# Optimization experiments

Measured on AMD Instinct MI355X. Metric: run time of the kernel, lower is better.

Reference implementation:

```python
import jax, jax.numpy as jnp
import numpy as np
from jax import lax

C = 256
HEADS = 8
HEAD_DIM = C // HEADS
B, H, W = 16, 32, 32
EPS = 1e-5


def conv3x3(x, w, b):
    # x: [B,C,H,W], w: [O,I,3,3]
    y = lax.conv_general_dilated(x, w, (1, 1), 'SAME',
                                 dimension_numbers=('NCHW', 'OIHW', 'NCHW'))
    return y + b[None, :, None, None]


def conv1x1(x, w, b):
    # w: [O,C]; pointwise conv as einsum
    return jnp.einsum('oc,bchw->bohw', w, x) + b[None, :, None, None]


def batchnorm(x, gamma, beta, mean, var):
    inv = gamma / jnp.sqrt(var + EPS)
    return x * inv[None, :, None, None] + (beta - mean * inv)[None, :, None, None]


def setup_inputs() -> dict:
    key = jax.random.key(0)
    ks = jax.random.split(key, 16)
    s3 = 1.0 / np.sqrt(C * 9)
    s1 = 1.0 / np.sqrt(C)
    return {
        'x': jax.random.normal(ks[0], (B, C, H, W), jnp.float32),
        'conv1_w': jax.random.normal(ks[1], (C, C, 3, 3), jnp.float32) * s3,
        'conv1_b': jnp.zeros((C,), jnp.float32),
        'bn1_gamma': jnp.ones((C,), jnp.float32),
        'bn1_beta': jnp.zeros((C,), jnp.float32),
        'bn1_mean': jax.random.normal(ks[2], (C,), jnp.float32) * 0.1,
        'bn1_var': jax.random.uniform(ks[3], (C,), jnp.float32, 0.5, 1.5),
        'conv2_w': jax.random.normal(ks[4], (C, C, 3, 3), jnp.float32) * s3,
        'conv2_b': jnp.zeros((C,), jnp.float32),
        'bn2_gamma': jnp.ones((C,), jnp.float32),
        'bn2_beta': jnp.zeros((C,), jnp.float32),
        'bn2_mean': jax.random.normal(ks[5], (C,), jnp.float32) * 0.1,
        'bn2_var': jax.random.uniform(ks[6], (C,), jnp.float32, 0.5, 1.5),
        'q_w': jax.random.normal(ks[7], (C, C), jnp.float32) * s1,
        'q_b': jnp.zeros((C,), jnp.float32),
        'k_w': jax.random.normal(ks[8], (C, C), jnp.float32) * s1,
        'k_b': jnp.zeros((C,), jnp.float32),
        'v_w': jax.random.normal(ks[9], (C, C), jnp.float32) * s1,
        'v_b': jnp.zeros((C,), jnp.float32),
        'out_w': jax.random.normal(ks[10], (C, C), jnp.float32) * s1,
        'out_b': jnp.zeros((C,), jnp.float32),
        'gate': jnp.asarray(0.1, jnp.float32),
    }


def reference(x, conv1_w, conv1_b, bn1_gamma, bn1_beta, bn1_mean, bn1_var,
              conv2_w, conv2_b, bn2_gamma, bn2_beta, bn2_mean, bn2_var,
              q_w, q_b, k_w, k_b, v_w, v_b, out_w, out_b, gate):
    b, c, h, w = x.shape
    n = h * w
    residual = x
    # conv residual path
    conv_out = jax.nn.relu(batchnorm(conv3x3(x, conv1_w, conv1_b),
                                     bn1_gamma, bn1_beta, bn1_mean, bn1_var))
    conv_out = batchnorm(conv3x3(conv_out, conv2_w, conv2_b),
                         bn2_gamma, bn2_beta, bn2_mean, bn2_var)
    # spatial multi-head attention (eval mode: dropout is identity)
    q = conv1x1(x, q_w, q_b).reshape(b, HEADS, HEAD_DIM, n)
    k = conv1x1(x, k_w, k_b).reshape(b, HEADS, HEAD_DIM, n)
    v = conv1x1(x, v_w, v_b).reshape(b, HEADS, HEAD_DIM, n)
    scores = jnp.einsum('bhdn,bhdm->bhnm', q, k) / np.sqrt(HEAD_DIM).astype(np.float32)
    attn = jax.nn.softmax(scores, axis=-1)  # [B,heads,N,N]
    attn_out = jnp.einsum('bhdm,bhnm->bhdn', v, attn).reshape(b, c, h, w)
    attn_out = conv1x1(attn_out, out_w, out_b)
    out = conv_out + jax.nn.sigmoid(gate) * attn_out + residual
    return jax.nn.relu(out)
```

## Files before the change

kernel.cpp:

```cpp
#include <hip/hip_runtime.h>
#include <hip/hip_bf16.h>

using bf16 = __hip_bfloat16;
typedef __attribute__((ext_vector_type(4))) float floatx4;
typedef __attribute__((ext_vector_type(8))) __bf16 bf16x8;
typedef __attribute__((ext_vector_type(4))) __bf16 bf16x4;

#define LGKM_WAIT() asm volatile("s_waitcnt lgkmcnt(0)" ::: "memory")

__device__ __forceinline__ void prep_one(const float* __restrict__ src,
                                         bf16* __restrict__ dst, int idx, int ntaps)
{
    const int kk = idx & 31, o = (idx >> 5) & 255, kc = (idx >> 13) & 7, t = idx >> 16;
    dst[idx] = __float2bfloat16(src[(o * 256 + kc * 32 + kk) * ntaps + t]);
}

__global__ __launch_bounds__(256) void prep_all(
    const float* __restrict__ x, const float* __restrict__ w1,
    const float* __restrict__ qw, const float* __restrict__ kw,
    const float* __restrict__ vw, const float* __restrict__ ow,
    bf16* __restrict__ xk, bf16* __restrict__ w1f,
    bf16* __restrict__ qwf, bf16* __restrict__ kwf,
    bf16* __restrict__ vwf, bf16* __restrict__ owf)
{
    __shared__ float T[64][65];
    const int blk = blockIdx.x, tid = threadIdx.x;
    if (blk < 1024) {
        const int n0 = (blk & 15) * 64, c0 = ((blk >> 4) & 3) * 64, b = blk >> 6;
        #pragma unroll
        for (int it = 0; it < 4; ++it) {
            const int tau = tid + it * 256;
            const int c = tau >> 4, seg = tau & 15;
            const float4 vv = *(const float4*)&x[((b * 256 + c0 + c) << 10) + n0 + seg * 4];
            T[seg * 4 + 0][c] = vv.x; T[seg * 4 + 1][c] = vv.y;
            T[seg * 4 + 2][c] = vv.z; T[seg * 4 + 3][c] = vv.w;
        }
        __syncthreads();
        #pragma unroll
        for (int it = 0; it < 2; ++it) {
            const int tau = tid + it * 256;
            const int n = tau >> 3, seg = tau & 7;
            bf16x8 o8;
            #pragma unroll
            for (int q = 0; q < 8; ++q) o8[q] = (__bf16)T[n][seg * 8 + q];
            const int c = c0 + seg * 8;
            *(bf16x8*)&xk[((((b << 3) + (c >> 5)) << 10) + n0 + n) * 32 + (c & 31)] = o8;
        }
    } else if (blk < 1600) {
        const int base = (blk - 1024) * 1024 + tid;
        #pragma unroll
        for (int k = 0; k < 4; ++k) prep_one(w1, w1f, base + k * 256, 9);
    } else {
        const int r = (blk - 1600) * 256 + tid;
        prep_one(qw, qwf, r, 1);
        prep_one(kw, kwf, r, 1);
        prep_one(vw, vwf, r, 1);
        prep_one(ow, owf, r, 1);
    }
}

template<int MODE>
__device__ __forceinline__ void conv_body(
    unsigned char* smb, int bn, int bo, int b,
    const bf16* __restrict__ Wf, const bf16* __restrict__ Act,
    const float* __restrict__ bias,
    const float* __restrict__ gam, const float* __restrict__ bet,
    const float* __restrict__ mu, const float* __restrict__ var,
    void* __restrict__ outp)
{
    const int tid = threadIdx.x;
    const int wave = tid >> 6, lane = tid & 63;
    const int quad = lane >> 4, l16 = lane & 15;
    const int wm = wave & 1, wn = wave >> 1;

    int srow[4], scol[4], sn[4]; bool sval[4];
    #pragma unroll
    for (int it = 0; it < 4; ++it) {
        const int s = tid + it * 256;
        const int row = s >> 2;
        const int yi = row / 34, x34 = row - yi * 34;
        const int gy = bn * 4 - 1 + yi, gx = x34 - 1;
        sval[it] = (s < 816) & (gy >= 0) & (gy < 32) & (gx >= 0) & (gx < 32);
        sn[it] = (gy << 5) + gx;
        srow[it] = row; scol[it] = (s & 3) * 8;
    }

    const bf16* __restrict__ act0 = Act + ((size_t)b << 18);
    bf16x8 rg[4];
    #pragma unroll
    for (int it = 0; it < 4; ++it) {
        bf16x8 v = {};
        if (sval[it]) v = *(const bf16x8*)&act0[sn[it] * 32 + scol[it]];
        rg[it] = v;
    }
    {
        bf16* st = (bf16*)smb;
        #pragma unroll
        for (int it = 0; it < 4; ++it)
            if (tid + it * 256 < 816) *(bf16x8*)&st[srow[it] * 40 + scol[it]] = rg[it];
    }
    __syncthreads();

    floatx4 acc[4][2] = {};

    for (int kc = 0; kc < 8; ++kc) {
        if (kc < 7) {
            const bf16* __restrict__ actn = act0 + ((kc + 1) << 15);
            #pragma unroll
            for (int it = 0; it < 4; ++it) {
                bf16x8 v = {};
                if (sval[it]) v = *(const bf16x8*)&actn[sn[it] * 32 + scol[it]];
                rg[it] = v;
            }
        }
        const bf16* __restrict__ cur = (const bf16*)(smb + (kc & 1) * 16320);
        #pragma unroll
        for (int t = 0; t < 9; ++t) {
            const int dy = t / 3 - 1, dx = t % 3 - 1;
            bf16x8 af[4], wf[2];
            #pragma unroll
            for (int p = 0; p < 4; ++p) {
                const int m = wm * 64 + p * 16 + l16;
                const int row = ((m >> 5) + 1 + dy) * 34 + ((m & 31) + 1 + dx);
                af[p] = *(const bf16x8*)&cur[row * 40 + quad * 8];
            }
            #pragma unroll
            for (int p = 0; p < 2; ++p)
                wf[p] = *(const bf16x8*)&Wf[((((t * 8 + kc) << 8) + bo * 64 + wn * 32 + p * 16 + l16) << 5) + quad * 8];
            #pragma unroll
            for (int i = 0; i < 4; ++i)
                #pragma unroll
                for (int j = 0; j < 2; ++j)
                    acc[i][j] = __builtin_amdgcn_mfma_f32_16x16x32_bf16(af[i], wf[j], acc[i][j], 0, 0, 0);
        }
        if (kc < 7) {
            bf16* nxt = (bf16*)(smb + ((kc + 1) & 1) * 16320);
            #pragma unroll
            for (int it = 0; it < 4; ++it)
                if (tid + it * 256 < 816) *(bf16x8*)&nxt[srow[it] * 40 + scol[it]] = rg[it];
        }
        __syncthreads();
    }

    if constexpr (MODE == 0) {
        bf16* rp = (bf16*)(smb + wave * 5120);
        #pragma unroll
        for (int i = 0; i < 4; ++i)
            #pragma unroll
            for (int j = 0; j < 2; ++j) {
                const int oc = bo * 64 + wn * 32 + j * 16 + l16;
                const float inv = gam[oc] * rsqrtf(var[oc] + 1e-5f);
                const float sh = bet[oc] - mu[oc] * inv;
                const float bs = bias[oc];
                #pragma unroll
                for (int r = 0; r < 4; ++r) {
                    const float v = (acc[i][j][r] + bs) * inv + sh;
                    rp[(i * 16 + quad * 4 + r) * 40 + j * 16 + l16] =
                        __float2bfloat16(v < 0.0f ? 0.0f : v);
                }
            }
        LGKM_WAIT();
        const int kc2 = bo * 2 + wn;
        bf16* dst = (bf16*)outp + ((((size_t)b << 3) + kc2) << 15) + (bn * 128 + wm * 64) * 32;
        #pragma unroll
        for (int it = 0; it < 4; ++it) {
            const int s = it * 64 + lane;
            const int nl = s >> 2, cp = (s & 3) * 8;
            *(bf16x8*)&dst[nl * 32 + cp] = *(const bf16x8*)&rp[nl * 40 + cp];
        }
    } else {
        float* rp = (float*)(smb + wave * 8704);
        #pragma unroll
        for (int i = 0; i < 4; ++i)
            #pragma unroll
            for (int j = 0; j < 2; ++j) {
                const int oc = bo * 64 + wn * 32 + j * 16 + l16;
                const float inv = gam[oc] * rsqrtf(var[oc] + 1e-5f);
                const float sh = bet[oc] - mu[oc] * inv;
                const float bs = bias[oc];
                float4 o;
                o.x = (acc[i][j][0] + bs) * inv + sh;
                o.y = (acc[i][j][1] + bs) * inv + sh;
                o.z = (acc[i][j][2] + bs) * inv + sh;
                o.w = (acc[i][j][3] + bs) * inv + sh;
                *(float4*)&rp[(j * 16 + l16) * 68 + i * 16 + quad * 4] = o;
            }
        LGKM_WAIT();
        const int n0 = bn * 128 + wm * 64;
        #pragma unroll
        for (int it = 0; it < 8; ++it) {
            const int s = it * 64 + lane;
            const int ocl = s >> 4, nch = s & 15;
            const int oc = bo * 64 + wn * 32 + ocl;
            float4 v = *(const float4*)&rp[ocl * 68 + nch * 4];
            *(float4*)&((float*)outp)[((b * 256 + oc) << 10) + n0 + nch * 4] = v;
        }
    }
}

__device__ __forceinline__ void qkv_body(
    unsigned char* qsm, int bn, int by, int b,
    const bf16* __restrict__ Wq, const bf16* __restrict__ Wk, const bf16* __restrict__ Wv,
    const bf16* __restrict__ Act,
    const float* __restrict__ bq, const float* __restrict__ bk, const float* __restrict__ bv,
    bf16* __restrict__ Oq, bf16* __restrict__ Ok, bf16* __restrict__ Ov, float qscale)
{
    const int sel = by >> 2, bo = by & 3;
    const bf16* __restrict__ Wf = (sel == 0) ? Wq : (sel == 1) ? Wk : Wv;
    const float* __restrict__ bias = (sel == 0) ? bq : (sel == 1) ? bk : bv;
    const float scale = (sel == 0) ? qscale : 1.0f;

    const int tid = threadIdx.x;
    const int wave = tid >> 6, lane = tid & 63;
    const int quad = lane >> 4, l16 = lane & 15;
    const int wm = wave & 1, wn = wave >> 1;

    floatx4 acc[4][2] = {};

    for (int kc = 0; kc < 8; ++kc) {
        const bf16* __restrict__ actk = Act + ((size_t)b << 18) + (kc << 15);
        bf16x8 af[4], wf[2];
        #pragma unroll
        for (int p = 0; p < 4; ++p)
            af[p] = *(const bf16x8*)&actk[(bn * 128 + wm * 64 + p * 16 + l16) * 32 + quad * 8];
        #pragma unroll
        for (int p = 0; p < 2; ++p)
            wf[p] = *(const bf16x8*)&Wf[(((kc << 8) + bo * 64 + wn * 32 + p * 16 + l16) << 5) + quad * 8];
        #pragma unroll
        for (int i = 0; i < 4; ++i)
            #pragma unroll
            for (int j = 0; j < 2; ++j)
                acc[i][j] = __builtin_amdgcn_mfma_f32_16x16x32_bf16(af[i], wf[j], acc[i][j], 0, 0, 0);
    }

    if (sel < 2) {
        bf16* rp = (bf16*)(qsm + wave * 5120);
        #pragma unroll
        for (int i = 0; i < 4; ++i)
            #pragma unroll
            for (int j = 0; j < 2; ++j) {
                const int oc = bo * 64 + wn * 32 + j * 16 + l16;
                const float bs = bias[oc];
                #pragma unroll
                for (int r = 0; r < 4; ++r)
                    rp[(i * 16 + quad * 4 + r) * 40 + j * 16 + l16] =
                        __float2bfloat16((acc[i][j][r] + bs) * scale);
            }
        LGKM_WAIT();
        bf16* __restrict__ outp = (sel == 0) ? Oq : Ok;
        const int h = bo * 2 + wn;
        bf16* dst = outp + ((((size_t)b << 3) + h) << 15) + (bn * 128 + wm * 64) * 32;
        #pragma unroll
        for (int it = 0; it < 4; ++it) {
            const int s = it * 64 + lane;
            const int nl = s >> 2, cp = (s & 3) * 8;
            *(bf16x8*)&dst[nl * 32 + cp] = *(const bf16x8*)&rp[nl * 40 + cp];
        }
    } else {
        #pragma unroll
        for (int i = 0; i < 4; ++i)
            #pragma unroll
            for (int j = 0; j < 2; ++j) {
                const int oc = bo * 64 + wn * 32 + j * 16 + l16;
                const int h = oc >> 5, d = oc & 31;
                const float bs = bias[oc];
                bf16x4 o4;
                #pragma unroll
                for (int r = 0; r < 4; ++r) o4[r] = (__bf16)(acc[i][j][r] + bs);
                const int key = bn * 128 + wm * 64 + i * 16 + quad * 4;
                *(bf16x4*)&Ov[(((((size_t)b << 3) + h) * 32 + (key >> 5)) * 32 + d) * 32 + (key & 31)] = o4;
            }
    }
}

__device__ __forceinline__ void attn_body(
    unsigned char* smb, int L,
    const bf16* __restrict__ Q, const bf16* __restrict__ K,
    const bf16* __restrict__ V, bf16* __restrict__ O)
{
    bf16 (*Pl)[32][136] = (bf16 (*)[32][136])smb;

    const int h = L & 7, slot = L >> 3;
    const int b = slot & 15, qb = slot >> 4;
    const int tid = threadIdx.x;
    const int wave = tid >> 6, lane = tid & 63;
    const int quad = lane >> 4, l16 = lane & 15;

    const bf16* __restrict__ Qh = Q + ((((size_t)b << 3) + h) << 15);
    const bf16* __restrict__ Kh = K + ((((size_t)b << 3) + h) << 15);
    const bf16* __restrict__ Vh = V + ((((size_t)b << 3) + h) << 15);
    const int qrow0 = qb * 128 + wave * 32;

    bf16x8 qf[2];
    #pragma unroll
    for (int i = 0; i < 2; ++i)
        qf[i] = *(const bf16x8*)&Qh[(qrow0 + i * 16 + l16) * 32 + quad * 8];

    float lp[2] = {0.0f, 0.0f};
    floatx4 oacc[2][2] = {};

    for (int kt = 0; kt < 8; ++kt) {
        bf16x8 kf[8];
        #pragma unroll
        for (int kb = 0; kb < 8; ++kb)
            kf[kb] = *(const bf16x8*)&Kh[(kt * 128 + kb * 16 + l16) * 32 + quad * 8];
        bf16x8 vb[2][4];
        #pragma unroll
        for (int jd = 0; jd < 2; ++jd)
            #pragma unroll
            for (int kk = 0; kk < 4; ++kk)
                vb[jd][kk] = *(const bf16x8*)&Vh[(((kt * 4 + kk) << 5) + jd * 16 + l16) * 32 + quad * 8];

        #pragma unroll
        for (int kb = 0; kb < 8; ++kb) {
            #pragma unroll
            for (int i = 0; i < 2; ++i) {
                floatx4 zz = {0.f, 0.f, 0.f, 0.f};
                floatx4 st = __builtin_amdgcn_mfma_f32_16x16x32_bf16(kf[kb], qf[i], zz, 0, 0, 0);
                const float e0 = __builtin_amdgcn_exp2f(st[0]);
                const float e1 = __builtin_amdgcn_exp2f(st[1]);
                const float e2 = __builtin_amdgcn_exp2f(st[2]);
                const float e3 = __builtin_amdgcn_exp2f(st[3]);
                lp[i] += (e0 + e1) + (e2 + e3);
                bf16x4 p4 = {(__bf16)e0, (__bf16)e1, (__bf16)e2, (__bf16)e3};
                *(bf16x4*)&Pl[wave][i * 16 + l16][kb * 16 + quad * 4] = p4;
            }
        }

        #pragma unroll
        for (int kk = 0; kk < 4; ++kk) {
            bf16x8 pf[2];
            #pragma unroll
            for (int i = 0; i < 2; ++i)
                pf[i] = *(const bf16x8*)&Pl[wave][i * 16 + l16][kk * 32 + quad * 8];
            #pragma unroll
            for (int jd = 0; jd < 2; ++jd)
                #pragma unroll
                for (int i = 0; i < 2; ++i)
                    oacc[jd][i] = __builtin_amdgcn_mfma_f32_16x16x32_bf16(
                        vb[jd][kk], pf[i], oacc[jd][i], 0, 0, 0);
        }
    }

    bf16* __restrict__ Oh = O + ((((size_t)b << 3) + h) << 15);
    #pragma unroll
    for (int i = 0; i < 2; ++i) {
        float l = lp[i];
        l += __shfl_xor(l, 16, 64);
        l += __shfl_xor(l, 32, 64);
        const float inv = 1.0f / l;
        const int qn = qrow0 + i * 16 + l16;
        #pragma unroll
        for (int jd = 0; jd < 2; ++jd) {
            bf16x4 o4;
            #pragma unroll
            for (int r = 0; r < 4; ++r) o4[r] = (__bf16)(oacc[jd][i][r] * inv);
            *(bf16x4*)&Oh[qn * 32 + jd * 16 + quad * 4] = o4;
        }
    }
}

__global__ __launch_bounds__(256) void phase1_k(
    const bf16* __restrict__ w1f, const bf16* __restrict__ xk,
    const float* __restrict__ cb1,
    const float* __restrict__ g1, const float* __restrict__ be1,
    const float* __restrict__ mu1, const float* __restrict__ va1,
    bf16* __restrict__ y1k,
    const bf16* __restrict__ qwf, const bf16* __restrict__ kwf, const bf16* __restrict__ vwf,
    const float* __restrict__ qb_, const float* __restrict__ kb_, const float* __restrict__ vb_,
    bf16* __restrict__ qT, bf16* __restrict__ kT, bf16* __restrict__ vbuf, float qscale,
    const float* __restrict__ w2, bf16* __restrict__ w2f)
{
    __shared__ __align__(16) unsigned char smb[34816];
    const int L = blockIdx.x;
    if (L < 512) {
        const int bn = L & 7, bo = (L >> 3) & 3, b = L >> 5;
        conv_body<0>(smb, bn, bo, b, w1f, xk, cb1, g1, be1, mu1, va1, (void*)y1k);
    } else if (L < 2048) {
        const int L2 = L - 512;
        const int bn = L2 & 7, by = (L2 >> 3) % 12, b = L2 / 96;
        qkv_body(smb, bn, by, b, qwf, kwf, vwf, xk, qb_, kb_, vb_, qT, kT, vbuf, qscale);
    } else {
        const int base = (L - 2048) * 1024 + threadIdx.x;
        #pragma unroll
        for (int k = 0; k < 4; ++k) prep_one(w2, w2f, base + k * 256, 9);
    }
}

__global__ __launch_bounds__(256) void phase2_k(
    const bf16* __restrict__ w2f, const bf16* __restrict__ y1k,
    const float* __restrict__ cb2,
    const float* __restrict__ g2, const float* __restrict__ be2,
    const float* __restrict__ mu2, const float* __restrict__ va2,
    float* __restrict__ c2,
    const bf16* __restrict__ qT, const bf16* __restrict__ kT,
    const bf16* __restrict__ vbuf, bf16* __restrict__ attnk)
{
    __shared__ __align__(16) unsigned char smb[34816];
    const int L = blockIdx.x;
    if (L < 512) {
        const int bn = L & 7, bo = (L >> 3) & 3, b = L >> 5;
        conv_body<1>(smb, bn, bo, b, w2f, y1k, cb2, g2, be2, mu2, va2, (void*)c2);
    } else {
        attn_body(smb, L - 512, qT, kT, vbuf, attnk);
    }
}

__global__ __launch_bounds__(256) void fi_k(
    const bf16* __restrict__ Wf, const bf16* __restrict__ Act,
    const float* __restrict__ bias,
    const float* __restrict__ c2, const float* __restrict__ resid,
    const float* __restrict__ gate, float* __restrict__ outp)
{
    __shared__ __align__(16) unsigned char fsm[34816];
    const int bn = blockIdx.x, bo = blockIdx.y, b = blockIdx.z;
    const int tid = threadIdx.x;
    const int wave = tid >> 6, lane = tid & 63;
    const int quad = lane >> 4, l16 = lane & 15;
    const int wm = wave & 1, wn = wave >> 1;

    floatx4 acc[4][2] = {};

    for (int kc = 0; kc < 8; ++kc) {
        const bf16* __restrict__ actk = Act + ((size_t)b << 18) + (kc << 15);
        bf16x8 af[4], wf[2];
        #pragma unroll
        for (int p = 0; p < 4; ++p)
            af[p] = *(const bf16x8*)&actk[(bn * 128 + wm * 64 + p * 16 + l16) * 32 + quad * 8];
        #pragma unroll
        for (int p = 0; p < 2; ++p)
            wf[p] = *(const bf16x8*)&Wf[(((kc << 8) + bo * 64 + wn * 32 + p * 16 + l16) << 5) + quad * 8];
        #pragma unroll
        for (int i = 0; i < 4; ++i)
            #pragma unroll
            for (int j = 0; j < 2; ++j)
                acc[i][j] = __builtin_amdgcn_mfma_f32_16x16x32_bf16(af[i], wf[j], acc[i][j], 0, 0, 0);
    }

    const float sg = 1.0f / (1.0f + __expf(-gate[0]));

    float* rp = (float*)(fsm + wave * 8704);
    #pragma unroll
    for (int i = 0; i < 4; ++i)
        #pragma unroll
        for (int j = 0; j < 2; ++j) {
            const int oc = bo * 64 + wn * 32 + j * 16 + l16;
            const float bs = bias[oc];
            float4 o;
            o.x = acc[i][j][0] + bs; o.y = acc[i][j][1] + bs;
            o.z = acc[i][j][2] + bs; o.w = acc[i][j][3] + bs;
            *(float4*)&rp[(j * 16 + l16) * 68 + i * 16 + quad * 4] = o;
        }
    LGKM_WAIT();
    const int n0 = bn * 128 + wm * 64;
    #pragma unroll
    for (int it = 0; it < 8; ++it) {
        const int s = it * 64 + lane;
        const int ocl = s >> 4, nch = s & 15;
        const int oc = bo * 64 + wn * 32 + ocl;
        const int idx = ((b * 256 + oc) << 10) + n0 + nch * 4;
        float4 v = *(const float4*)&rp[ocl * 68 + nch * 4];
        const float4 cc = *(const float4*)&c2[idx];
        const float4 rr = *(const float4*)&resid[idx];
        float4 o;
        o.x = cc.x + sg * v.x + rr.x; o.y = cc.y + sg * v.y + rr.y;
        o.z = cc.z + sg * v.z + rr.z; o.w = cc.w + sg * v.w + rr.w;
        o.x = o.x < 0.0f ? 0.0f : o.x; o.y = o.y < 0.0f ? 0.0f : o.y;
        o.z = o.z < 0.0f ? 0.0f : o.z; o.w = o.w < 0.0f ? 0.0f : o.w;
        *(float4*)&outp[idx] = o;
    }
}

extern "C" void kernel_launch(void* const* d_in, const int* in_sizes, int n_in,
                              void* d_out, int out_size, void* d_ws, size_t ws_size,
                              hipStream_t stream)
{
    const float* x    = (const float*)d_in[0];
    const float* w1   = (const float*)d_in[1];
    const float* cb1  = (const float*)d_in[2];
    const float* g1   = (const float*)d_in[3];
    const float* be1  = (const float*)d_in[4];
    const float* mu1  = (const float*)d_in[5];
    const float* va1  = (const float*)d_in[6];
    const float* w2   = (const float*)d_in[7];
    const float* cb2  = (const float*)d_in[8];
    const float* g2   = (const float*)d_in[9];
    const float* be2  = (const float*)d_in[10];
    const float* mu2  = (const float*)d_in[11];
    const float* va2  = (const float*)d_in[12];
    const float* qw   = (const float*)d_in[13];
    const float* qb_  = (const float*)d_in[14];
    const float* kw   = (const float*)d_in[15];
    const float* kb_  = (const float*)d_in[16];
    const float* vw   = (const float*)d_in[17];
    const float* vb_  = (const float*)d_in[18];
    const float* ow   = (const float*)d_in[19];
    const float* ob_  = (const float*)d_in[20];
    const float* gate = (const float*)d_in[21];

    char* ws = (char*)d_ws;
    bf16*  xk    = (bf16*) (ws + 0);
    bf16*  y1k   = (bf16*) (ws + 8388608);
    bf16*  attnk = (bf16*) (ws + 8388608);
    float* c2    = (float*)(ws + 16777216);
    bf16*  qT    = (bf16*) (ws + 33554432);
    bf16*  kT    = (bf16*) (ws + 41943040);
    bf16*  vbuf  = (bf16*) (ws + 50331648);
    bf16*  w1f   = (bf16*) (ws + 58720256);
    bf16*  w2f   = (bf16*) (ws + 59899904);
    bf16*  qwf   = (bf16*) (ws + 61079552);
    bf16*  kwf   = (bf16*) (ws + 61210624);
    bf16*  vwf   = (bf16*) (ws + 61341696);
    bf16*  owf   = (bf16*) (ws + 61472768);

    dim3 blk(256, 1, 1);
    prep_all<<<dim3(1856), blk, 0, stream>>>(x, w1, qw, kw, vw, ow,
                                             xk, w1f, qwf, kwf, vwf, owf);

    phase1_k<<<dim3(2624), blk, 0, stream>>>(w1f, xk, cb1, g1, be1, mu1, va1, y1k,
                                             qwf, kwf, vwf, qb_, kb_, vb_,
                                             qT, kT, vbuf, 0.2550392430300696f,
                                             w2, w2f);
    phase2_k<<<dim3(1536), blk, 0, stream>>>(w2f, y1k, cb2, g2, be2, mu2, va2, c2,
                                             qT, kT, vbuf, attnk);
    dim3 gg(8, 4, 16);
    fi_k<<<gg, blk, 0, stream>>>(owf, attnk, ob_, c2, x, gate, (float*)d_out);

    (void)in_sizes; (void)n_in; (void)out_size; (void)ws_size;
}
```

Before: 230.1 us.

## Use 32x32 MFMA in attention, store conv2 output as bf16, retile final kernel

The attention inner loop switches from 16x16x32 to 32x32x16 bf16 MFMA tiles. This lowers per-instruction overhead and the cost of K/V fragment loads and LDS traffic per score. The conv2 intermediate is now stored as bf16 instead of fp32, halving its write and read traffic, at some cost in precision before the residual add. The final fused output kernel uses smaller 64x64 tiles over 1024 blocks with an XCD-aware block remap, and attnk gets its own workspace slot instead of aliasing y1k.

```diff
diff --git a/kernel.cpp b/kernel.cpp
--- a/kernel.cpp
+++ b/kernel.cpp
@@ -3,10 +3,19 @@
 
 using bf16 = __hip_bfloat16;
 typedef __attribute__((ext_vector_type(4))) float floatx4;
+typedef __attribute__((ext_vector_type(16))) float floatx16;
 typedef __attribute__((ext_vector_type(8))) __bf16 bf16x8;
 typedef __attribute__((ext_vector_type(4))) __bf16 bf16x4;
 
 #define LGKM_WAIT() asm volatile("s_waitcnt lgkmcnt(0)" ::: "memory")
+
+__device__ __forceinline__ void remap1024(int L, int& bn, int& bo, int& b)
+{
+    const int xcd = L & 7, slot = L >> 3;
+    b  = (xcd << 1) | (slot & 1);
+    bo = (slot >> 1) & 3;
+    bn = slot >> 3;
+}
 
 __device__ __forceinline__ void prep_one(const float* __restrict__ src,
                                          bf16* __restrict__ dst, int idx, int ntaps)
@@ -66,7 +75,7 @@
     const float* __restrict__ bias,
     const float* __restrict__ gam, const float* __restrict__ bet,
     const float* __restrict__ mu, const float* __restrict__ var,
-    void* __restrict__ outp)
+    bf16* __restrict__ outp)
 {
     const int tid = threadIdx.x;
     const int wave = tid >> 6, lane = tid & 63;
@@ -161,7 +170,7 @@
             }
         LGKM_WAIT();
         const int kc2 = bo * 2 + wn;
-        bf16* dst = (bf16*)outp + ((((size_t)b << 3) + kc2) << 15) + (bn * 128 + wm * 64) * 32;
+        bf16* dst = outp + ((((size_t)b << 3) + kc2) << 15) + (bn * 128 + wm * 64) * 32;
         #pragma unroll
         for (int it = 0; it < 4; ++it) {
             const int s = it * 64 + lane;
@@ -169,7 +178,7 @@
             *(bf16x8*)&dst[nl * 32 + cp] = *(const bf16x8*)&rp[nl * 40 + cp];
         }
     } else {
-        float* rp = (float*)(smb + wave * 8704);
+        bf16* rp = (bf16*)(smb + wave * 4608);
         #pragma unroll
         for (int i = 0; i < 4; ++i)
             #pragma unroll
@@ -178,22 +187,21 @@
                 const float inv = gam[oc] * rsqrtf(var[oc] + 1e-5f);
                 const float sh = bet[oc] - mu[oc] * inv;
                 const float bs = bias[oc];
-                float4 o;
-                o.x = (acc[i][j][0] + bs) * inv + sh;
-                o.y = (acc[i][j][1] + bs) * inv + sh;
-                o.z = (acc[i][j][2] + bs) * inv + sh;
-                o.w = (acc[i][j][3] + bs) * inv + sh;
-                *(float4*)&rp[(j * 16 + l16) * 68 + i * 16 + quad * 4] = o;
+                bf16x4 o4;
+                #pragma unroll
+                for (int r = 0; r < 4; ++r)
+                    o4[r] = (__bf16)((acc[i][j][r] + bs) * inv + sh);
+                *(bf16x4*)&rp[(j * 16 + l16) * 72 + i * 16 + quad * 4] = o4;
             }
         LGKM_WAIT();
         const int n0 = bn * 128 + wm * 64;
         #pragma unroll
-        for (int it = 0; it < 8; ++it) {
+        for (int it = 0; it < 4; ++it) {
             const int s = it * 64 + lane;
-            const int ocl = s >> 4, nch = s & 15;
+            const int ocl = s >> 3, nch = s & 7;
             const int oc = bo * 64 + wn * 32 + ocl;
-            float4 v = *(const float4*)&rp[ocl * 68 + nch * 4];
-            *(float4*)&((float*)outp)[((b * 256 + oc) << 10) + n0 + nch * 4] = v;
+            *(bf16x8*)&outp[((b * 256 + oc) << 10) + n0 + nch * 8] =
+                *(const bf16x8*)&rp[ocl * 72 + nch * 8];
         }
     }
 }
@@ -284,7 +292,7 @@
     const int b = slot & 15, qb = slot >> 4;
     const int tid = threadIdx.x;
     const int wave = tid >> 6, lane = tid & 63;
-    const int quad = lane >> 4, l16 = lane & 15;
+    const int l31 = lane & 31, lh = lane >> 5;
 
     const bf16* __restrict__ Qh = Q + ((((size_t)b << 3) + h) << 15);
     const bf16* __restrict__ Kh = K + ((((size_t)b << 3) + h) << 15);
@@ -293,70 +301,54 @@
 
     bf16x8 qf[2];
     #pragma unroll
-    for (int i = 0; i < 2; ++i)
-        qf[i] = *(const bf16x8*)&Qh[(qrow0 + i * 16 + l16) * 32 + quad * 8];
-
-    float lp[2] = {0.0f, 0.0f};
-    floatx4 oacc[2][2] = {};
+    for (int ks = 0; ks < 2; ++ks)
+        qf[ks] = *(const bf16x8*)&Qh[(qrow0 + l31) * 32 + ks * 16 + lh * 8];
+
+    float lp = 0.0f;
+    floatx16 oacc = {};
 
     for (int kt = 0; kt < 8; ++kt) {
-        bf16x8 kf[8];
-        #pragma unroll
-        for (int kb = 0; kb < 8; ++kb)
-            kf[kb] = *(const bf16x8*)&Kh[(kt * 128 + kb * 16 + l16) * 32 + quad * 8];
-        bf16x8 vb[2][4];
-        #pragma unroll
-        for (int jd = 0; jd < 2; ++jd)
-            #pragma unroll
-            for (int kk = 0; kk < 4; ++kk)
-                vb[jd][kk] = *(const bf16x8*)&Vh[(((kt * 4 + kk) << 5) + jd * 16 + l16) * 32 + quad * 8];
-
-        #pragma unroll
-        for (int kb = 0; kb < 8; ++kb) {
-            #pragma unroll
-            for (int i = 0; i < 2; ++i) {
-                floatx4 zz = {0.f, 0.f, 0.f, 0.f};
-                floatx4 st = __builtin_amdgcn_mfma_f32_16x16x32_bf16(kf[kb], qf[i], zz, 0, 0, 0);
-                const float e0 = __builtin_amdgcn_exp2f(st[0]);
-                const float e1 = __builtin_amdgcn_exp2f(st[1]);
-                const float e2 = __builtin_amdgcn_exp2f(st[2]);
-                const float e3 = __builtin_amdgcn_exp2f(st[3]);
-                lp[i] += (e0 + e1) + (e2 + e3);
+        bf16x8 vf[8];
+        #pragma unroll
+        for (int ks = 0; ks < 8; ++ks)
+            vf[ks] = *(const bf16x8*)&Vh[((((kt << 2) + (ks >> 1)) << 5) + l31) * 32
+                                         + (ks & 1) * 16 + lh * 8];
+
+        #pragma unroll
+        for (int kb = 0; kb < 4; ++kb) {
+            bf16x8 ka0 = *(const bf16x8*)&Kh[(kt * 128 + kb * 32 + l31) * 32 + lh * 8];
+            bf16x8 ka1 = *(const bf16x8*)&Kh[(kt * 128 + kb * 32 + l31) * 32 + 16 + lh * 8];
+            floatx16 st = {};
+            st = __builtin_amdgcn_mfma_f32_32x32x16_bf16(ka0, qf[0], st, 0, 0, 0);
+            st = __builtin_amdgcn_mfma_f32_32x32x16_bf16(ka1, qf[1], st, 0, 0, 0);
+            #pragma unroll
+            for (int g = 0; g < 4; ++g) {
+                const float e0 = __builtin_amdgcn_exp2f(st[g * 4 + 0]);
+                const float e1 = __builtin_amdgcn_exp2f(st[g * 4 + 1]);
+                const float e2 = __builtin_amdgcn_exp2f(st[g * 4 + 2]);
+                const float e3 = __builtin_amdgcn_exp2f(st[g * 4 + 3]);
+                lp += (e0 + e1) + (e2 + e3);
                 bf16x4 p4 = {(__bf16)e0, (__bf16)e1, (__bf16)e2, (__bf16)e3};
-                *(bf16x4*)&Pl[wave][i * 16 + l16][kb * 16 + quad * 4] = p4;
-            }
-        }
-
-        #pragma unroll
-        for (int kk = 0; kk < 4; ++kk) {
-            bf16x8 pf[2];
-            #pragma unroll
-            for (int i = 0; i < 2; ++i)
-                pf[i] = *(const bf16x8*)&Pl[wave][i * 16 + l16][kk * 32 + quad * 8];
-            #pragma unroll
-            for (int jd = 0; jd < 2; ++jd)
-                #pragma unroll
-                for (int i = 0; i < 2; ++i)
-                    oacc[jd][i] = __builtin_amdgcn_mfma_f32_16x16x32_bf16(
-                        vb[jd][kk], pf[i], oacc[jd][i], 0, 0, 0);
-        }
-    }
-
+                *(bf16x4*)&Pl[wave][l31][kb * 32 + g * 8 + lh * 4] = p4;
+            }
+        }
+
+        #pragma unroll
+        for (int ks = 0; ks < 8; ++ks) {
+            bf16x8 pf = *(const bf16x8*)&Pl[wave][l31][ks * 16 + lh * 8];
+            oacc = __builtin_amdgcn_mfma_f32_32x32x16_bf16(vf[ks], pf, oacc, 0, 0, 0);
+        }
+    }
+
+    lp += __shfl_xor(lp, 32, 64);
+    const float inv = 1.0f / lp;
     bf16* __restrict__ Oh = O + ((((size_t)b << 3) + h) << 15);
     #pragma unroll
-    for (int i = 0; i < 2; ++i) {
-        float l = lp[i];
-        l += __shfl_xor(l, 16, 64);
-        l += __shfl_xor(l, 32, 64);
-        const float inv = 1.0f / l;
-        const int qn = qrow0 + i * 16 + l16;
-        #pragma unroll
-        for (int jd = 0; jd < 2; ++jd) {
-            bf16x4 o4;
-            #pragma unroll
-            for (int r = 0; r < 4; ++r) o4[r] = (__bf16)(oacc[jd][i][r] * inv);
-            *(bf16x4*)&Oh[qn * 32 + jd * 16 + quad * 4] = o4;
-        }
+    for (int g = 0; g < 4; ++g) {
+        bf16x4 o4;
+        #pragma unroll
+        for (int r = 0; r < 4; ++r) o4[r] = (__bf16)(oacc[g * 4 + r] * inv);
+        *(bf16x4*)&Oh[(qrow0 + l31) * 32 + g * 8 + lh * 4] = o4;
     }
 }
 
@@ -375,7 +367,7 @@
     const int L = blockIdx.x;
     if (L < 512) {
         const int bn = L & 7, bo = (L >> 3) & 3, b = L >> 5;
-        conv_body<0>(smb, bn, bo, b, w1f, xk, cb1, g1, be1, mu1, va1, (void*)y1k);
+        conv_body<0>(smb, bn, bo, b, w1f, xk, cb1, g1, be1, mu1, va1, y1k);
     } else if (L < 2048) {
         const int L2 = L - 512;
         const int bn = L2 & 7, by = (L2 >> 3) % 12, b = L2 / 96;
@@ -392,7 +384,7 @@
     const float* __restrict__ cb2,
     const float* __restrict__ g2, const float* __restrict__ be2,
     const float* __restrict__ mu2, const float* __restrict__ va2,
-    float* __restrict__ c2,
+    bf16* __restrict__ c2b,
     const bf16* __restrict__ qT, const bf16* __restrict__ kT,
     const bf16* __restrict__ vbuf, bf16* __restrict__ attnk)
 {
@@ -400,7 +392,7 @@
     const int L = blockIdx.x;
     if (L < 512) {
         const int bn = L & 7, bo = (L >> 3) & 3, b = L >> 5;
-        conv_body<1>(smb, bn, bo, b, w2f, y1k, cb2, g2, be2, mu2, va2, (void*)c2);
+        conv_body<1>(smb, bn, bo, b, w2f, y1k, cb2, g2, be2, mu2, va2, c2b);
     } else {
         attn_body(smb, L - 512, qT, kT, vbuf, attnk);
     }
@@ -409,29 +401,29 @@
 __global__ __launch_bounds__(256) void fi_k(
     const bf16* __restrict__ Wf, const bf16* __restrict__ Act,
     const float* __restrict__ bias,
-    const float* __restrict__ c2, const float* __restrict__ resid,
+    const bf16* __restrict__ c2b, const float* __restrict__ resid,
     const float* __restrict__ gate, float* __restrict__ outp)
 {
-    __shared__ __align__(16) unsigned char fsm[34816];
-    const int bn = blockIdx.x, bo = blockIdx.y, b = blockIdx.z;
+    __shared__ __align__(16) unsigned char fsm[18432];
+    int bn, bo, b; remap1024(blockIdx.x, bn, bo, b);
     const int tid = threadIdx.x;
     const int wave = tid >> 6, lane = tid & 63;
     const int quad = lane >> 4, l16 = lane & 15;
     const int wm = wave & 1, wn = wave >> 1;
 
-    floatx4 acc[4][2] = {};
+    floatx4 acc[2][2] = {};
 
     for (int kc = 0; kc < 8; ++kc) {
         const bf16* __restrict__ actk = Act + ((size_t)b << 18) + (kc << 15);
-        bf16x8 af[4], wf[2];
-        #pragma unroll
-        for (int p = 0; p < 4; ++p)
-            af[p] = *(const bf16x8*)&actk[(bn * 128 + wm * 64 + p * 16 + l16) * 32 + quad * 8];
+        bf16x8 af[2], wf[2];
+        #pragma unroll
+        for (int p = 0; p < 2; ++p)
+            af[p] = *(const bf16x8*)&actk[(bn * 64 + wm * 32 + p * 16 + l16) * 32 + quad * 8];
         #pragma unroll
         for (int p = 0; p < 2; ++p)
             wf[p] = *(const bf16x8*)&Wf[(((kc << 8) + bo * 64 + wn * 32 + p * 16 + l16) << 5) + quad * 8];
         #pragma unroll
-        for (int i = 0; i < 4; ++i)
+        for (int i = 0; i < 2; ++i)
             #pragma unroll
             for (int j = 0; j < 2; ++j)
                 acc[i][j] = __builtin_amdgcn_mfma_f32_16x16x32_bf16(af[i], wf[j], acc[i][j], 0, 0, 0);
@@ -439,9 +431,9 @@
 
     const float sg = 1.0f / (1.0f + __expf(-gate[0]));
 
-    float* rp = (float*)(fsm + wave * 8704);
+    float* rp = (float*)(fsm + wave * 4608);
     #pragma unroll
-    for (int i = 0; i < 4; ++i)
+    for (int i = 0; i < 2; ++i)
         #pragma unroll
         for (int j = 0; j < 2; ++j) {
             const int oc = bo * 64 + wn * 32 + j * 16 + l16;
@@ -449,22 +441,24 @@
             float4 o;
             o.x = acc[i][j][0] + bs; o.y = acc[i][j][1] + bs;
             o.z = acc[i][j][2] + bs; o.w = acc[i][j][3] + bs;
-            *(float4*)&rp[(j * 16 + l16) * 68 + i * 16 + quad * 4] = o;
+            *(float4*)&rp[(j * 16 + l16) * 36 + i * 16 + quad * 4] = o;
         }
     LGKM_WAIT();
-    const int n0 = bn * 128 + wm * 64;
+    const int n0 = bn * 64 + wm * 32;
     #pragma unroll
-    for (int it = 0; it < 8; ++it) {
+    for (int it = 0; it < 4; ++it) {
         const int s = it * 64 + lane;
-        const int ocl = s >> 4, nch = s & 15;
+        const int ocl = s >> 3, nch = s & 7;
         const int oc = bo * 64 + wn * 32 + ocl;
         const int idx = ((b * 256 + oc) << 10) + n0 + nch * 4;
-        float4 v = *(const float4*)&rp[ocl * 68 + nch * 4];
-        const float4 cc = *(const float4*)&c2[idx];
+        float4 v = *(const float4*)&rp[ocl * 36 + nch * 4];
+        const bf16x4 ccb = *(const bf16x4*)&c2b[idx];
         const float4 rr = *(const float4*)&resid[idx];
         float4 o;
-        o.x = cc.x + sg * v.x + rr.x; o.y = cc.y + sg * v.y + rr.y;
-        o.z = cc.z + sg * v.z + rr.z; o.w = cc.w + sg * v.w + rr.w;
+        o.x = (float)ccb[0] + sg * v.x + rr.x;
+        o.y = (float)ccb[1] + sg * v.y + rr.y;
+        o.z = (float)ccb[2] + sg * v.z + rr.z;
+        o.w = (float)ccb[3] + sg * v.w + rr.w;
         o.x = o.x < 0.0f ? 0.0f : o.x; o.y = o.y < 0.0f ? 0.0f : o.y;
         o.z = o.z < 0.0f ? 0.0f : o.z; o.w = o.w < 0.0f ? 0.0f : o.w;
         *(float4*)&outp[idx] = o;
@@ -501,8 +495,8 @@
     char* ws = (char*)d_ws;
     bf16*  xk    = (bf16*) (ws + 0);
     bf16*  y1k   = (bf16*) (ws + 8388608);
-    bf16*  attnk = (bf16*) (ws + 8388608);
-    float* c2    = (float*)(ws + 16777216);
+    bf16*  c2b   = (bf16*) (ws + 16777216);
+    bf16*  attnk = (bf16*) (ws + 25165824);
     bf16*  qT    = (bf16*) (ws + 33554432);
     bf16*  kT    = (bf16*) (ws + 41943040);
     bf16*  vbuf  = (bf16*) (ws + 50331648);
@@ -521,10 +515,9 @@
                                              qwf, kwf, vwf, qb_, kb_, vb_,
                                              qT, kT, vbuf, 0.2550392430300696f,
                                              w2, w2f);
-    phase2_k<<<dim3(1536), blk, 0, stream>>>(w2f, y1k, cb2, g2, be2, mu2, va2, c2,
+    phase2_k<<<dim3(1536), blk, 0, stream>>>(w2f, y1k, cb2, g2, be2, mu2, va2, c2b,
                                              qT, kT, vbuf, attnk);
-    dim3 gg(8, 4, 16);
-    fi_k<<<gg, blk, 0, stream>>>(owf, attnk, ob_, c2, x, gate, (float*)d_out);
+    fi_k<<<dim3(1024), blk, 0, stream>>>(owf, attnk, ob_, c2b, x, gate, (float*)d_out);
 
     (void)in_sizes; (void)n_in; (void)out_size; (void)ws_size;
 }
```

After: 228.8 us. No clear change (-0.5%).
